# Kernel tuning notes

Measured on AMD Instinct MI355X. Metric: run time of the kernel, lower is better.

The kernel has to match this reference:

```python
import jax, jax.numpy as jnp
import numpy as np

N, K, D, H = 100000, 16, 128, 4
HD = D // H
EPS = 1e-5


def layer_norm(x, g, b):
    mu = jnp.mean(x, axis=-1, keepdims=True)
    var = jnp.mean(jnp.square(x - mu), axis=-1, keepdims=True)
    return (x - mu) * jax.lax.rsqrt(var + EPS) * g + b


def setup_inputs() -> dict:
    key = jax.random.key(0)
    ks = jax.random.split(key, 8)
    s = 0.02
    x = jax.random.normal(ks[0], (N, D), jnp.float32)
    attention_samples = jax.random.randint(ks[1], (N, K), 0, N)
    in_proj_w = jax.random.normal(ks[2], (3 * D, D), jnp.float32) * s
    in_proj_b = jnp.zeros((3 * D,), jnp.float32)
    out_w = jax.random.normal(ks[3], (D, D), jnp.float32) * s
    out_b = jnp.zeros((D,), jnp.float32)
    ffn_w1 = jax.random.normal(ks[4], (4 * D, D), jnp.float32) * s
    ffn_b1 = jnp.zeros((4 * D,), jnp.float32)
    ffn_w2 = jax.random.normal(ks[5], (D, 4 * D), jnp.float32) * s
    ffn_b2 = jnp.zeros((D,), jnp.float32)
    ln1_g = jnp.ones((D,), jnp.float32)
    ln1_b = jnp.zeros((D,), jnp.float32)
    ln2_g = jnp.ones((D,), jnp.float32)
    ln2_b = jnp.zeros((D,), jnp.float32)
    return dict(x=x, attention_samples=attention_samples, in_proj_w=in_proj_w,
                in_proj_b=in_proj_b, out_w=out_w, out_b=out_b,
                ffn_w1=ffn_w1, ffn_b1=ffn_b1, ffn_w2=ffn_w2, ffn_b2=ffn_b2,
                ln1_g=ln1_g, ln1_b=ln1_b, ln2_g=ln2_g, ln2_b=ln2_b)


def reference(x, attention_samples, in_proj_w, in_proj_b, out_w, out_b,
              ffn_w1, ffn_b1, ffn_w2, ffn_b2, ln1_g, ln1_b, ln2_g, ln2_b):
    n = x.shape[0]
    k = attention_samples.shape[1]
    wq, wk, wv = in_proj_w[:D], in_proj_w[D:2 * D], in_proj_w[2 * D:]
    bq, bk, bv = in_proj_b[:D], in_proj_b[D:2 * D], in_proj_b[2 * D:]
    # Project first (one [N,D] GEMM each), then gather the projections.
    # Mathematically identical to torch's gather-then-project (projection is per-row linear).
    q = x @ wq.T + bq                      # [N, D]
    kx = x @ wk.T + bk                     # [N, D]
    vx = x @ wv.T + bv                     # [N, D]
    k_s = kx[attention_samples]            # [N, K, D]
    v_s = vx[attention_samples]            # [N, K, D]
    qh = q.reshape(n, H, HD)               # [N, H, HD]
    kh = k_s.reshape(n, k, H, HD)          # [N, K, H, HD]
    vh = v_s.reshape(n, k, H, HD)
    scores = jnp.einsum('nhd,nkhd->nhk', qh, kh) / np.sqrt(HD).astype(np.float32)
    w = jax.nn.softmax(scores, axis=-1)    # [N, H, K]
    attn = jnp.einsum('nhk,nkhd->nhd', w, vh).reshape(n, D)
    attn = attn @ out_w.T + out_b          # out_proj
    x = layer_norm(x + attn, ln1_g, ln1_b)
    h = jax.nn.relu(x @ ffn_w1.T + ffn_b1)
    x = layer_norm(x + h @ ffn_w2.T + ffn_b2, ln2_g, ln2_b)
    return x
```

## Files before the change

kernel.cpp:

```cpp
#include <hip/hip_runtime.h>
#include <hip/hip_bf16.h>
#include <hip/hip_fp8.h>

#define NTOK 100000
#define EPS 1e-5f

using frag  = __attribute__((ext_vector_type(8))) short;
using f32x4 = __attribute__((ext_vector_type(4))) float;
typedef __hip_bfloat16 bf16;
typedef unsigned short ushort_t;

__device__ inline float bits2f(unsigned int u) { union { unsigned int i; float f; } x; x.i = u; return x.f; }
__device__ inline void bfu_unpack(unsigned int u, float& lo, float& hi) {
  lo = bits2f(u << 16);
  hi = bits2f(u & 0xffff0000u);
}

__device__ inline float4 fp8x4_to_f4(unsigned int u) {
  __hip_fp8_e4m3 a, b, c, d;
  a.__x = u & 0xff; b.__x = (u >> 8) & 0xff; c.__x = (u >> 16) & 0xff; d.__x = (u >> 24) & 0xff;
  return make_float4((float)a, (float)b, (float)c, (float)d);
}
__device__ inline unsigned char f_to_fp8(float f) { __hip_fp8_e4m3 t(f); return t.__x; }

__global__ __launch_bounds__(256) void cvt_x_kernel(const float* __restrict__ in,
                                                    bf16* __restrict__ out) {
  const int e = (blockIdx.x * 256 + threadIdx.x) * 4;
  float4 v = *(const float4*)&in[e];
  bf16 o[4] = {__float2bfloat16(v.x), __float2bfloat16(v.y),
               __float2bfloat16(v.z), __float2bfloat16(v.w)};
  *(ulong1*)&out[e] = *(ulong1*)o;
}

__global__ __launch_bounds__(256) void cvt_w_kernel(
    const float* __restrict__ w0, const float* __restrict__ w1,
    const float* __restrict__ w2, const float* __restrict__ w3,
    bf16* __restrict__ out) {
  const int e = (blockIdx.x * 256 + threadIdx.x) * 4;
  const float* src;
  int off;
  if (e < 49152)       { src = w0; off = 0; }
  else if (e < 65536)  { src = w1; off = 49152; }
  else if (e < 131072) { src = w2; off = 65536; }
  else                 { src = w3; off = 131072; }
  float4 v = *(const float4*)&src[e - off];
  bf16 o[4] = {__float2bfloat16(v.x), __float2bfloat16(v.y),
               __float2bfloat16(v.z), __float2bfloat16(v.w)};
  *(ulong1*)&out[e] = *(ulong1*)o;
}

template<int KSTEPS>
__device__ __forceinline__ void gemm_body(
    const bf16* __restrict__ A,
    const bf16* __restrict__ Wslab,
    int row0, int M, ushort_t* Bs, f32x4 (&acc)[2][8]) {
  const int KTOT = KSTEPS * 128;
  const int tid = threadIdx.x;
  const int lane = tid & 63;
  const int lr = lane & 15, kg = lane >> 4;

  int r0 = row0 + lr;      if (r0 > M - 1) r0 = M - 1;
  int r1 = row0 + 16 + lr; if (r1 > M - 1) r1 = M - 1;
  const bf16* a0 = A + (size_t)r0 * KTOT + kg * 8;
  const bf16* a1 = A + (size_t)r1 * KTOT + kg * 8;

  frag a[2][4];
#pragma unroll
  for (int kc = 0; kc < 4; ++kc) {
    a[0][kc] = *(const frag*)(a0 + kc * 32);
    a[1][kc] = *(const frag*)(a1 + kc * 32);
  }

  uint4 sreg[8];
#pragma unroll
  for (int r = 0; r < 8; ++r) {
    const int g = r * 256 + tid, row = g >> 4, u = g & 15;
    sreg[r] = *(const uint4*)(Wslab + (size_t)row * KTOT + (u ^ (row & 15)) * 8);
  }
#pragma unroll
  for (int r = 0; r < 8; ++r) {
    const int g = r * 256 + tid, row = g >> 4, u = g & 15;
    *(uint4*)&Bs[row * 128 + u * 8] = sreg[r];
  }
  __syncthreads();

#pragma unroll
  for (int kc = 0; kc < 4; ++kc) {
    const int uoff = ((kc * 4 + kg) ^ lr) * 8;
#pragma unroll
    for (int j = 0; j < 8; ++j) {
      frag b = *(const frag*)&Bs[(lr + 16 * j) * 128 + uoff];
      acc[0][j] = __builtin_amdgcn_mfma_f32_16x16x32_bf16(a[0][kc], b, acc[0][j], 0, 0, 0);
      acc[1][j] = __builtin_amdgcn_mfma_f32_16x16x32_bf16(a[1][kc], b, acc[1][j], 0, 0, 0);
    }
  }
}

__global__ __launch_bounds__(256, 4) void k_qkv(
    const bf16* __restrict__ A, const bf16* __restrict__ W,
    const float* __restrict__ bias, bf16* __restrict__ qout,
    unsigned char* __restrict__ kout, unsigned char* __restrict__ vout, int M) {
  __shared__ ushort_t Bs[16384];
  const int lane = threadIdx.x & 63;
  const int wid = threadIdx.x >> 6;
  const int row0 = blockIdx.x * 128 + wid * 32;
  const int cbase = blockIdx.y * 128;
  const int lr = lane & 15, kg = lane >> 4;

  f32x4 acc[2][8] = {};
  gemm_body<1>(A, W + (size_t)cbase * 128, row0, M, Bs, acc);

  float bs[8];
#pragma unroll
  for (int j = 0; j < 8; ++j) bs[j] = bias[cbase + lr + 16 * j];
  const int y = blockIdx.y;
  unsigned char* f8dst = (y == 1) ? kout : vout;
#pragma unroll
  for (int i = 0; i < 2; ++i)
#pragma unroll
    for (int r = 0; r < 4; ++r) {
      const int row = row0 + 16 * i + 4 * kg + r;
      if (row >= M) continue;
      if (y == 0) {
        bf16* orow = qout + (size_t)row * 128 + lr;
#pragma unroll
        for (int j = 0; j < 8; ++j) orow[16 * j] = __float2bfloat16(acc[i][j][r] + bs[j]);
      } else {
        unsigned char* orow = f8dst + (size_t)row * 128 + lr;
#pragma unroll
        for (int j = 0; j < 8; ++j) orow[16 * j] = f_to_fp8(acc[i][j][r] + bs[j]);
      }
    }
}

__global__ __launch_bounds__(256, 4) void k_ffn1(
    const bf16* __restrict__ A, const bf16* __restrict__ W,
    const float* __restrict__ bias, bf16* __restrict__ out, int M) {
  __shared__ ushort_t Bs[16384];
  const int lane = threadIdx.x & 63;
  const int wid = threadIdx.x >> 6;
  const int row0 = blockIdx.x * 128 + wid * 32;
  const int cbase = blockIdx.y * 128;
  const int lr = lane & 15, kg = lane >> 4;

  f32x4 acc[2][8] = {};
  gemm_body<1>(A, W + (size_t)cbase * 128, row0, M, Bs, acc);

  float bs[8];
#pragma unroll
  for (int j = 0; j < 8; ++j) bs[j] = bias[cbase + lr + 16 * j];
#pragma unroll
  for (int i = 0; i < 2; ++i)
#pragma unroll
    for (int r = 0; r < 4; ++r) {
      const int row = row0 + 16 * i + 4 * kg + r;
      if (row >= M) continue;
      bf16* orow = out + (size_t)row * 512 + cbase + lr;
#pragma unroll
      for (int j = 0; j < 8; ++j)
        orow[16 * j] = __float2bfloat16(fmaxf(acc[i][j][r] + bs[j], 0.f));
    }
}

__global__ __launch_bounds__(256, 4) void k_outproj_ln(
    const bf16* __restrict__ A, const bf16* __restrict__ W,
    const float* __restrict__ bias, const bf16* __restrict__ resid,
    const float* __restrict__ g, const float* __restrict__ b,
    bf16* __restrict__ out, int M) {
  __shared__ ushort_t Bs[16384];
  const int lane = threadIdx.x & 63;
  const int wid = threadIdx.x >> 6;
  const int row0 = blockIdx.x * 128 + wid * 32;
  const int lr = lane & 15, kg = lane >> 4;

  f32x4 acc[2][8] = {};
  gemm_body<1>(A, W, row0, M, Bs, acc);

  float bs[8], gs[8], bbs[8];
#pragma unroll
  for (int j = 0; j < 8; ++j) {
    const int c = lr + 16 * j;
    bs[j] = bias[c]; gs[j] = g[c]; bbs[j] = b[c];
  }
#pragma unroll
  for (int i = 0; i < 2; ++i)
#pragma unroll
    for (int r = 0; r < 4; ++r) {
      const int row = row0 + 16 * i + 4 * kg + r;
      const int rr = (row > M - 1) ? (M - 1) : row;
      const bf16* rrow = resid + (size_t)rr * 128 + lr;
      float v[8], psum = 0.f, psq = 0.f;
#pragma unroll
      for (int j = 0; j < 8; ++j) {
        v[j] = acc[i][j][r] + bs[j] + __bfloat162float(rrow[16 * j]);
        psum += v[j];
        psq += v[j] * v[j];
      }
#pragma unroll
      for (int off = 1; off < 16; off <<= 1) {
        psum += __shfl_xor(psum, off);
        psq += __shfl_xor(psq, off);
      }
      const float mean = psum * (1.f / 128.f);
      const float var = psq * (1.f / 128.f) - mean * mean;
      const float rstd = rsqrtf(var + EPS);
      if (row < M) {
        bf16* orow = out + (size_t)row * 128 + lr;
#pragma unroll
        for (int j = 0; j < 8; ++j)
          orow[16 * j] = __float2bfloat16((v[j] - mean) * rstd * gs[j] + bbs[j]);
      }
    }
}

__global__ __launch_bounds__(256, 3) void k_ffn2_ln(
    const bf16* __restrict__ A,
    const bf16* __restrict__ W,
    const float* __restrict__ bias, const bf16* __restrict__ resid,
    const float* __restrict__ g, const float* __restrict__ b,
    float* __restrict__ out, int M) {
  __shared__ ushort_t Bs[16384];
  const int tid = threadIdx.x;
  const int lane = tid & 63;
  const int wid = tid >> 6;
  const int row0 = blockIdx.x * 128 + wid * 32;
  const int lr = lane & 15, kg = lane >> 4;
  const int rb = tid >> 4;
  const int uu = tid & 15;
  const int su = uu ^ rb;

  int r0 = row0 + lr;      if (r0 > M - 1) r0 = M - 1;
  int r1 = row0 + 16 + lr; if (r1 > M - 1) r1 = M - 1;
  const bf16* a0 = A + (size_t)r0 * 512 + kg * 8;
  const bf16* a1 = A + (size_t)r1 * 512 + kg * 8;
  const bf16* bgp = W + (size_t)rb * 512 + su * 8;
  const int lslot = rb * 128 + uu * 8;

  f32x4 acc[2][8] = {};
  frag aC0[4], aC1[4], aN0[4], aN1[4];
  uint4 sreg[8];

#define LDA(d0, d1, c)                                            \
  { _Pragma("unroll") for (int kc = 0; kc < 4; ++kc) {            \
      d0[kc] = *(const frag*)(a0 + (c) * 128 + kc * 32);          \
      d1[kc] = *(const frag*)(a1 + (c) * 128 + kc * 32); } }
#define LDB(c)                                                    \
  { _Pragma("unroll") for (int r = 0; r < 8; ++r)                 \
      sreg[r] = *(const uint4*)(bgp + (size_t)r * 16 * 512 + (c) * 128); }
#define WRB()                                                     \
  { _Pragma("unroll") for (int r = 0; r < 8; ++r)                 \
      *(uint4*)&Bs[lslot + r * 2048] = sreg[r]; }
#define STEP(s0, s1)                                              \
  { _Pragma("unroll") for (int kc = 0; kc < 4; ++kc) {            \
      const int uo = ((kc * 4 + kg) ^ lr) * 8;                    \
      _Pragma("unroll") for (int j = 0; j < 8; ++j) {             \
        frag bb = *(const frag*)&Bs[(lr + 16 * j) * 128 + uo];    \
        acc[0][j] = __builtin_amdgcn_mfma_f32_16x16x32_bf16(s0[kc], bb, acc[0][j], 0, 0, 0); \
        acc[1][j] = __builtin_amdgcn_mfma_f32_16x16x32_bf16(s1[kc], bb, acc[1][j], 0, 0, 0); } } }

  LDA(aC0, aC1, 0); LDB(0);
  WRB(); __syncthreads();

  LDA(aN0, aN1, 1); LDB(1);
  STEP(aC0, aC1);
  __syncthreads(); WRB(); __syncthreads();

  LDA(aC0, aC1, 2); LDB(2);
  STEP(aN0, aN1);
  __syncthreads(); WRB(); __syncthreads();

  LDA(aN0, aN1, 3); LDB(3);
  STEP(aC0, aC1);
  __syncthreads(); WRB(); __syncthreads();

  STEP(aN0, aN1);
#undef LDA
#undef LDB
#undef WRB
#undef STEP

  float bs[8], gs[8], bbs[8];
#pragma unroll
  for (int j = 0; j < 8; ++j) {
    const int c = lr + 16 * j;
    bs[j] = bias[c]; gs[j] = g[c]; bbs[j] = b[c];
  }
#pragma unroll
  for (int i = 0; i < 2; ++i)
#pragma unroll
    for (int r = 0; r < 4; ++r) {
      const int row = row0 + 16 * i + 4 * kg + r;
      const int rr = (row > M - 1) ? (M - 1) : row;
      const bf16* rrow = resid + (size_t)rr * 128 + lr;
      float v[8], psum = 0.f, psq = 0.f;
#pragma unroll
      for (int j = 0; j < 8; ++j) {
        v[j] = acc[i][j][r] + bs[j] + __bfloat162float(rrow[16 * j]);
        psum += v[j];
        psq += v[j] * v[j];
      }
#pragma unroll
      for (int off = 1; off < 16; off <<= 1) {
        psum += __shfl_xor(psum, off);
        psq += __shfl_xor(psq, off);
      }
      const float mean = psum * (1.f / 128.f);
      const float var = psq * (1.f / 128.f) - mean * mean;
      const float rstd = rsqrtf(var + EPS);
      if (row < M) {
        float* orow = out + (size_t)row * 128 + lr;
#pragma unroll
        for (int j = 0; j < 8; ++j)
          orow[16 * j] = (v[j] - mean) * rstd * gs[j] + bbs[j];
      }
    }
}

__global__ __launch_bounds__(256) void attn_kernel(
    const bf16* __restrict__ qb, const unsigned char* __restrict__ kf8,
    const unsigned char* __restrict__ vf8, const int* __restrict__ samples,
    bf16* __restrict__ attn) {
  const int lane = threadIdx.x & 63;
  const int wid = threadIdx.x >> 6;
  const int tok = blockIdx.x * 4 + wid;
  if (tok >= NTOK) return;
  const int qt = lane >> 4;
  const int lr = lane & 15;

  const float scale = 0.17677669529663687f;
  float q8[8];
  {
    uint4 qu = *(const uint4*)&qb[(size_t)tok * 128 + 8 * lr];
    bfu_unpack(qu.x, q8[0], q8[1]);
    bfu_unpack(qu.y, q8[2], q8[3]);
    bfu_unpack(qu.z, q8[4], q8[5]);
    bfu_unpack(qu.w, q8[6], q8[7]);
#pragma unroll
    for (int d = 0; d < 8; ++d) q8[d] *= scale;
  }

  const int myidx = samples[tok * 16 + lr];
  int kidx[4];
#pragma unroll
  for (int jj = 0; jj < 4; ++jj) kidx[jj] = __shfl(myidx, 4 * jj + qt, 16);

  float s[4];
#pragma unroll
  for (int jj = 0; jj < 4; ++jj) {
    uint2 ku = *(const uint2*)&kf8[(size_t)kidx[jj] * 128 + 8 * lr];
    float4 k0 = fp8x4_to_f4(ku.x), k1 = fp8x4_to_f4(ku.y);
    float p = q8[0] * k0.x + q8[1] * k0.y + q8[2] * k0.z + q8[3] * k0.w +
              q8[4] * k1.x + q8[5] * k1.y + q8[6] * k1.z + q8[7] * k1.w;
    p += __shfl_xor(p, 1);
    p += __shfl_xor(p, 2);
    s[jj] = p;
  }

  float m = fmaxf(fmaxf(s[0], s[1]), fmaxf(s[2], s[3]));
  m = fmaxf(m, __shfl_xor(m, 16));
  m = fmaxf(m, __shfl_xor(m, 32));
  float sum = 0.f;
#pragma unroll
  for (int jj = 0; jj < 4; ++jj) {
    s[jj] = __expf(s[jj] - m);
    sum += s[jj];
  }
  sum += __shfl_xor(sum, 16);
  sum += __shfl_xor(sum, 32);
  const float inv = 1.f / sum;

  float a8[8] = {};
#pragma unroll
  for (int jj = 0; jj < 4; ++jj) {
    uint2 vu = *(const uint2*)&vf8[(size_t)kidx[jj] * 128 + 8 * lr];
    float4 v0 = fp8x4_to_f4(vu.x), v1 = fp8x4_to_f4(vu.y);
    const float wj = s[jj] * inv;
    a8[0] += wj * v0.x; a8[1] += wj * v0.y; a8[2] += wj * v0.z; a8[3] += wj * v0.w;
    a8[4] += wj * v1.x; a8[5] += wj * v1.y; a8[6] += wj * v1.z; a8[7] += wj * v1.w;
  }
#pragma unroll
  for (int d = 0; d < 8; ++d) {
    a8[d] += __shfl_xor(a8[d], 16);
    a8[d] += __shfl_xor(a8[d], 32);
  }

  if (qt == 0) {
    uint4 o;
    o.x = (unsigned)__bfloat16_as_ushort(__float2bfloat16(a8[0])) |
          ((unsigned)__bfloat16_as_ushort(__float2bfloat16(a8[1])) << 16);
    o.y = (unsigned)__bfloat16_as_ushort(__float2bfloat16(a8[2])) |
          ((unsigned)__bfloat16_as_ushort(__float2bfloat16(a8[3])) << 16);
    o.z = (unsigned)__bfloat16_as_ushort(__float2bfloat16(a8[4])) |
          ((unsigned)__bfloat16_as_ushort(__float2bfloat16(a8[5])) << 16);
    o.w = (unsigned)__bfloat16_as_ushort(__float2bfloat16(a8[6])) |
          ((unsigned)__bfloat16_as_ushort(__float2bfloat16(a8[7])) << 16);
    *(uint4*)&attn[(size_t)tok * 128 + 8 * lr] = o;
  }
}

extern "C" void kernel_launch(void* const* d_in, const int* in_sizes, int n_in,
                              void* d_out, int out_size, void* d_ws, size_t ws_size,
                              hipStream_t stream) {
  const float* x      = (const float*)d_in[0];
  const int* samples  = (const int*)d_in[1];
  const float* in_w   = (const float*)d_in[2];
  const float* in_b   = (const float*)d_in[3];
  const float* out_w  = (const float*)d_in[4];
  const float* out_b  = (const float*)d_in[5];
  const float* ffn_w1 = (const float*)d_in[6];
  const float* ffn_b1 = (const float*)d_in[7];
  const float* ffn_w2 = (const float*)d_in[8];
  const float* ffn_b2 = (const float*)d_in[9];
  const float* ln1_g  = (const float*)d_in[10];
  const float* ln1_b  = (const float*)d_in[11];
  const float* ln2_g  = (const float*)d_in[12];
  const float* ln2_b  = (const float*)d_in[13];
  float* out = (float*)d_out;

  char* ws = (char*)d_ws;
  bf16* xb   = (bf16*)(ws);
  bf16* qb   = (bf16*)(ws + 25600000);
  unsigned char* kf8 = (unsigned char*)(ws + 51200000);
  unsigned char* vf8 = (unsigned char*)(ws + 64000000);
  bf16* attn = (bf16*)(ws + 76800000);
  bf16* h    = (bf16*)(ws);
  bf16* x1b  = (bf16*)(ws + 102400000);
  bf16* wb   = (bf16*)(ws + 128000000);
  bf16* in_wb   = wb;
  bf16* out_wb  = wb + 49152;
  bf16* ffn_w1b = wb + 65536;
  bf16* ffn_w2b = wb + 131072;

  const int M = NTOK;
  dim3 blk(256);
  const int gm = (M + 127) / 128;

  cvt_x_kernel<<<dim3(12500), blk, 0, stream>>>(x, xb);
  cvt_w_kernel<<<dim3(192), blk, 0, stream>>>(in_w, out_w, ffn_w1, ffn_w2, wb);
  k_qkv<<<dim3(gm, 3), blk, 0, stream>>>(xb, in_wb, in_b, qb, kf8, vf8, M);
  attn_kernel<<<dim3((M + 3) / 4), blk, 0, stream>>>(qb, kf8, vf8, samples, attn);
  k_outproj_ln<<<dim3(gm), blk, 0, stream>>>(attn, out_wb, out_b, xb, ln1_g, ln1_b, x1b, M);
  k_ffn1<<<dim3(gm, 4), blk, 0, stream>>>(x1b, ffn_w1b, ffn_b1, h, M);
  k_ffn2_ln<<<dim3(gm), blk, 0, stream>>>(h, ffn_w2b, ffn_b2, x1b, ln2_g, ln2_b, out, M);
}
```

Baseline: 226.3 us.

## Stage weight tiles via direct global-to-LDS loads and double-buffer FFN2 weights

Result: faster. 196.9 us (-13.0%).

```diff
diff --git a/kernel.cpp b/kernel.cpp
--- a/kernel.cpp
+++ b/kernel.cpp
@@ -22,6 +22,11 @@
   return make_float4((float)a, (float)b, (float)c, (float)d);
 }
 __device__ inline unsigned char f_to_fp8(float f) { __hip_fp8_e4m3 t(f); return t.__x; }
+
+#define GL_LDS16(gsrc, ldst)                                                  \
+  __builtin_amdgcn_global_load_lds(                                           \
+      (const __attribute__((address_space(1))) void*)(gsrc),                  \
+      (__attribute__((address_space(3))) void*)(ldst), 16, 0, 0)
 
 __global__ __launch_bounds__(256) void cvt_x_kernel(const float* __restrict__ in,
                                                     bf16* __restrict__ out) {
@@ -49,20 +54,27 @@
   *(ulong1*)&out[e] = *(ulong1*)o;
 }
 
-template<int KSTEPS>
-__device__ __forceinline__ void gemm_body(
-    const bf16* __restrict__ A,
-    const bf16* __restrict__ Wslab,
+__device__ __forceinline__ void stage_B(const bf16* __restrict__ Wslab, int KTOT,
+                                        int c, ushort_t* Bs, int tid) {
+#pragma unroll
+  for (int r = 0; r < 8; ++r) {
+    const int g = r * 256 + tid, row = g >> 4, u = g & 15;
+    GL_LDS16(Wslab + (size_t)row * KTOT + (size_t)c * 128 + (u ^ (row & 15)) * 8,
+             Bs + g * 8);
+  }
+}
+
+__device__ __forceinline__ void gemm_body128(
+    const bf16* __restrict__ A, const bf16* __restrict__ Wslab,
     int row0, int M, ushort_t* Bs, f32x4 (&acc)[2][8]) {
-  const int KTOT = KSTEPS * 128;
   const int tid = threadIdx.x;
   const int lane = tid & 63;
   const int lr = lane & 15, kg = lane >> 4;
 
   int r0 = row0 + lr;      if (r0 > M - 1) r0 = M - 1;
   int r1 = row0 + 16 + lr; if (r1 > M - 1) r1 = M - 1;
-  const bf16* a0 = A + (size_t)r0 * KTOT + kg * 8;
-  const bf16* a1 = A + (size_t)r1 * KTOT + kg * 8;
+  const bf16* a0 = A + (size_t)r0 * 128 + kg * 8;
+  const bf16* a1 = A + (size_t)r1 * 128 + kg * 8;
 
   frag a[2][4];
 #pragma unroll
@@ -70,18 +82,7 @@
     a[0][kc] = *(const frag*)(a0 + kc * 32);
     a[1][kc] = *(const frag*)(a1 + kc * 32);
   }
-
-  uint4 sreg[8];
-#pragma unroll
-  for (int r = 0; r < 8; ++r) {
-    const int g = r * 256 + tid, row = g >> 4, u = g & 15;
-    sreg[r] = *(const uint4*)(Wslab + (size_t)row * KTOT + (u ^ (row & 15)) * 8);
-  }
-#pragma unroll
-  for (int r = 0; r < 8; ++r) {
-    const int g = r * 256 + tid, row = g >> 4, u = g & 15;
-    *(uint4*)&Bs[row * 128 + u * 8] = sreg[r];
-  }
+  stage_B(Wslab, 128, 0, Bs, tid);
   __syncthreads();
 
 #pragma unroll
@@ -108,7 +109,7 @@
   const int lr = lane & 15, kg = lane >> 4;
 
   f32x4 acc[2][8] = {};
-  gemm_body<1>(A, W + (size_t)cbase * 128, row0, M, Bs, acc);
+  gemm_body128(A, W + (size_t)cbase * 128, row0, M, Bs, acc);
 
   float bs[8];
 #pragma unroll
@@ -144,7 +145,7 @@
   const int lr = lane & 15, kg = lane >> 4;
 
   f32x4 acc[2][8] = {};
-  gemm_body<1>(A, W + (size_t)cbase * 128, row0, M, Bs, acc);
+  gemm_body128(A, W + (size_t)cbase * 128, row0, M, Bs, acc);
 
   float bs[8];
 #pragma unroll
@@ -174,7 +175,7 @@
   const int lr = lane & 15, kg = lane >> 4;
 
   f32x4 acc[2][8] = {};
-  gemm_body<1>(A, W, row0, M, Bs, acc);
+  gemm_body128(A, W, row0, M, Bs, acc);
 
   float bs[8], gs[8], bbs[8];
 #pragma unroll
@@ -213,70 +214,61 @@
     }
 }
 
-__global__ __launch_bounds__(256, 3) void k_ffn2_ln(
+__global__ __launch_bounds__(256, 2) void k_ffn2_ln(
     const bf16* __restrict__ A,
     const bf16* __restrict__ W,
     const float* __restrict__ bias, const bf16* __restrict__ resid,
     const float* __restrict__ g, const float* __restrict__ b,
     float* __restrict__ out, int M) {
-  __shared__ ushort_t Bs[16384];
+  __shared__ ushort_t Bs0[16384];
+  __shared__ ushort_t Bs1[16384];
   const int tid = threadIdx.x;
   const int lane = tid & 63;
   const int wid = tid >> 6;
   const int row0 = blockIdx.x * 128 + wid * 32;
   const int lr = lane & 15, kg = lane >> 4;
-  const int rb = tid >> 4;
-  const int uu = tid & 15;
-  const int su = uu ^ rb;
 
   int r0 = row0 + lr;      if (r0 > M - 1) r0 = M - 1;
   int r1 = row0 + 16 + lr; if (r1 > M - 1) r1 = M - 1;
   const bf16* a0 = A + (size_t)r0 * 512 + kg * 8;
   const bf16* a1 = A + (size_t)r1 * 512 + kg * 8;
-  const bf16* bgp = W + (size_t)rb * 512 + su * 8;
-  const int lslot = rb * 128 + uu * 8;
 
   f32x4 acc[2][8] = {};
   frag aC0[4], aC1[4], aN0[4], aN1[4];
-  uint4 sreg[8];
 
 #define LDA(d0, d1, c)                                            \
   { _Pragma("unroll") for (int kc = 0; kc < 4; ++kc) {            \
       d0[kc] = *(const frag*)(a0 + (c) * 128 + kc * 32);          \
       d1[kc] = *(const frag*)(a1 + (c) * 128 + kc * 32); } }
-#define LDB(c)                                                    \
-  { _Pragma("unroll") for (int r = 0; r < 8; ++r)                 \
-      sreg[r] = *(const uint4*)(bgp + (size_t)r * 16 * 512 + (c) * 128); }
-#define WRB()                                                     \
-  { _Pragma("unroll") for (int r = 0; r < 8; ++r)                 \
-      *(uint4*)&Bs[lslot + r * 2048] = sreg[r]; }
-#define STEP(s0, s1)                                              \
+#define STEP(B, s0, s1)                                           \
   { _Pragma("unroll") for (int kc = 0; kc < 4; ++kc) {            \
       const int uo = ((kc * 4 + kg) ^ lr) * 8;                    \
       _Pragma("unroll") for (int j = 0; j < 8; ++j) {             \
-        frag bb = *(const frag*)&Bs[(lr + 16 * j) * 128 + uo];    \
+        frag bb = *(const frag*)&B[(lr + 16 * j) * 128 + uo];     \
         acc[0][j] = __builtin_amdgcn_mfma_f32_16x16x32_bf16(s0[kc], bb, acc[0][j], 0, 0, 0); \
         acc[1][j] = __builtin_amdgcn_mfma_f32_16x16x32_bf16(s1[kc], bb, acc[1][j], 0, 0, 0); } } }
 
-  LDA(aC0, aC1, 0); LDB(0);
-  WRB(); __syncthreads();
-
-  LDA(aN0, aN1, 1); LDB(1);
-  STEP(aC0, aC1);
-  __syncthreads(); WRB(); __syncthreads();
-
-  LDA(aC0, aC1, 2); LDB(2);
-  STEP(aN0, aN1);
-  __syncthreads(); WRB(); __syncthreads();
-
-  LDA(aN0, aN1, 3); LDB(3);
-  STEP(aC0, aC1);
-  __syncthreads(); WRB(); __syncthreads();
-
-  STEP(aN0, aN1);
+  LDA(aC0, aC1, 0);
+  stage_B(W, 512, 0, Bs0, tid);
+  __syncthreads();
+
+  LDA(aN0, aN1, 1);
+  stage_B(W, 512, 1, Bs1, tid);
+  STEP(Bs0, aC0, aC1);
+  __syncthreads();
+
+  LDA(aC0, aC1, 2);
+  stage_B(W, 512, 2, Bs0, tid);
+  STEP(Bs1, aN0, aN1);
+  __syncthreads();
+
+  LDA(aN0, aN1, 3);
+  stage_B(W, 512, 3, Bs1, tid);
+  STEP(Bs0, aC0, aC1);
+  __syncthreads();
+
+  STEP(Bs1, aN0, aN1);
 #undef LDA
-#undef LDB
-#undef WRB
 #undef STEP
 
   float bs[8], gs[8], bbs[8];
```
